# Kernel optimization log

Measured on AMD Instinct MI355X. Metric: run time of the kernel, lower is better.

The kernel has to match this reference:

```python
import jax, jax.numpy as jnp
import numpy as np

B, S, D = 2048, 200, 128  # batch, history length, embedding dim
H = 64                    # attention_units[0]

def setup_inputs() -> dict:
    key = jax.random.key(0)
    k1, k2, k3, k4, k5 = jax.random.split(key, 5)
    return {
        "target_item": jax.random.normal(k1, (B, D), dtype=jnp.float32),
        "history_sequence": jax.random.normal(k2, (B, S, D), dtype=jnp.float32),
        "mask": jax.random.randint(k3, (B, S), 0, 2, dtype=jnp.int32),
        "W1": jax.random.normal(k4, (4 * D, H), dtype=jnp.float32) * (1.0 / np.sqrt(4 * D)),
        "b1": jnp.zeros((H,), dtype=jnp.float32),
        "W2": jax.random.normal(k5, (H, 1), dtype=jnp.float32) * (1.0 / np.sqrt(H)),
        "b2": jnp.zeros((1,), dtype=jnp.float32),
    }

def reference(target_item, history_sequence, mask, W1, b1, W2, b2):
    b, s, d = history_sequence.shape
    t = jnp.broadcast_to(target_item[:, None, :], (b, s, d))  # [B,S,D]
    # concat(target, history, diff, product) -> [B,S,4D]
    x = jnp.concatenate(
        [t, history_sequence, t - history_sequence, t * history_sequence], axis=-1)
    h = jax.nn.relu(x @ W1 + b1)          # [B,S,H]
    w = (h @ W2 + b2)[..., 0]             # [B,S]
    m = mask.astype(w.dtype)
    w = w * m                              # zero out padded positions (pre-softmax, as in source)
    w = w + (-1e9) * (1.0 - m)             # mask for softmax
    w = jax.nn.softmax(w, axis=-1)
    return jnp.einsum('bs,bsd->bd', w, history_sequence)  # [B,D]
```

## Files before the change

### kernel.cpp

```cpp
#include <hip/hip_runtime.h>
#include <hip/hip_bf16.h>

typedef __attribute__((ext_vector_type(8))) short bf16x8;
typedef __attribute__((ext_vector_type(4))) float f32x4;

#define B_ 2048
#define S_ 200
#define D_ 128
#define H_ 64
#define LOG2E 1.44269504f
#define TR 16
#define TB 8192

#define WS_AC 0u
#define WS_WB 32768u

static __device__ __forceinline__ short f2bf_hw(float f) {
    return (short)__builtin_bit_cast(unsigned short, __float2bfloat16(f));
}

static __device__ __forceinline__ void gload16(const void* g, void* l) {
    __builtin_amdgcn_global_load_lds(
        (const __attribute__((address_space(1))) unsigned int*)g,
        (__attribute__((address_space(3))) unsigned int*)l, 16, 0, 0);
}

__global__ __launch_bounds__(128)
void prep_fold(const float* __restrict__ W1, char* __restrict__ ws)
{
    const int n = blockIdx.x;
    const int k = threadIdx.x;
    float a = W1[k * H_ + n];
    float b = W1[(128 + k) * H_ + n];
    float c = W1[(256 + k) * H_ + n];
    float d = W1[(384 + k) * H_ + n];
    ((float*)(ws + WS_AC))[k * 64 + n] = a + c;
    char* img = ws + WS_WB;
    const int sw = (n & 7) << 4;
    const int kk = k >> 3, e2 = (k & 7) * 2;
    *(short*)(img + n * 512 + ((kk * 16) ^ sw) + e2)        = f2bf_hw(b - c);
    *(short*)(img + n * 512 + (((16 + kk) * 16) ^ sw) + e2) = f2bf_hw(d);
}

__global__ __launch_bounds__(256) __attribute__((amdgpu_waves_per_eu(1, 1)))
void din_fused(const float* __restrict__ tgt, const float* __restrict__ hist,
               const int* __restrict__ mask, const float* __restrict__ W2,
               const float* __restrict__ b1, const char* __restrict__ ws,
               float* __restrict__ out)
{
    __shared__ __align__(16) char L[139264];
    const int tid  = threadIdx.x;
    const int lane = tid & 63;
    const int wv   = tid >> 6;
    const int b    = blockIdx.x * 4 + wv;
    const int lo   = lane & 15;
    const int hi   = lane >> 4;
    char* Lm = L + 32768 + wv * 26624;

    {
        const char* wsrc = ws + WS_WB + wv * 8192 + (size_t)lane * 16u;
        #pragma unroll
        for (int i = 0; i < 8; ++i)
            gload16(wsrc + i * 1024, L + wv * 8192 + i * 1024);
    }

    f32x4 w2v[4];
    #pragma unroll
    for (int ng = 0; ng < 4; ++ng) {
        f32x4 wl = *(const f32x4*)(W2 + ng * 16 + hi * 4);
        w2v[ng] = (f32x4){wl[0] * LOG2E, wl[1] * LOG2E, wl[2] * LOG2E, wl[3] * LOG2E};
    }
    f32x4 tp0[4], tp1[4];
    #pragma unroll
    for (int ks = 0; ks < 4; ++ks) {
        tp0[ks] = *(const f32x4*)(tgt + (size_t)b * D_ + ks * 32 + hi * 8);
        tp1[ks] = *(const f32x4*)(tgt + (size_t)b * D_ + ks * 32 + hi * 8 + 4);
    }

    int* lst = (int*)(Lm + 1024);
    int cnt = 0, uni = 0;
    {
        const int* mp = mask + (size_t)b * S_;
        int last = 0;
        #pragma unroll
        for (int c = 0; c < 4; ++c) {
            int s = c * 64 + lane;
            int m = (s < S_) ? mp[s] : 0;
            unsigned long long bal = __ballot(m != 0);
            if (m) lst[cnt + __builtin_popcountll(bal & ((1ull << lane) - 1ull))] = s;
            if (bal) last = c * 64 + (63 - __builtin_clzll(bal));
            cnt += __builtin_popcountll(bal);
        }
        if (cnt == 0) { uni = 1; cnt = S_; }
        for (int p = cnt + lane; p < 208; p += 64) lst[p] = uni ? (S_ - 1) : last;
        if (uni)
            for (int p = lane; p < S_; p += 64) lst[p] = p;
    }

    {
        const float* ak = (const float*)(ws + WS_AC) + lane;
        const float* tb = tgt + (size_t)b * D_;
        float ta = 0.f;
        #pragma unroll 16
        for (int d = 0; d < 128; ++d)
            ta = fmaf(tb[d], ak[d * 64], ta);
        ta += b1[lane];
        *(float*)(Lm + 512 + lane * 4) = ta;
    }
    f32x4 tav[4];
    #pragma unroll
    for (int ng = 0; ng < 4; ++ng)
        tav[ng] = *(const f32x4*)(Lm + 512 + (ng * 16 + hi * 4) * 4);

    asm volatile("s_waitcnt vmcnt(0)" ::: "memory");
    __syncthreads();

    const int nt = (cnt + 15) >> 4;
    const int* ll = (const int*)(Lm + 1024);

    int abase[4], akoff[8];
    #pragma unroll
    for (int ng = 0; ng < 4; ++ng) abase[ng] = (ng * 16 + lo) * 512;
    #pragma unroll
    for (int ks = 0; ks < 8; ++ks) akoff[ks] = (ks * 64 + hi * 16) ^ ((lo & 7) << 4);
    bf16x8 bfH[4][4];
    #pragma unroll
    for (int ks = 0; ks < 4; ++ks)
        #pragma unroll
        for (int ng = 0; ng < 4; ++ng)
            bfH[ks][ng] = *(const bf16x8*)(L + abase[ng] + akoff[ks]);

    const int rb = (lo * 512 + hi * 32) ^ ((lo & 7) << 4);
    char* BB0 = Lm + 2048;
    char* BB1 = Lm + 2048 + TB;
    char* BB2 = Lm + 2048 + 2 * TB;

    const char* hb = (const char*)hist + (size_t)b * (S_ * D_ * 4);
    const int cp = (lane & 31) * 16;
    const int h5 = lane >> 5;
    auto stage = [&](int t, char* bufp) {
        #pragma unroll
        for (int i = 0; i < 8; ++i) {
            int r = 2 * i + h5;
            int rr = ll[t * 16 + r];
            gload16(hb + (size_t)rr * 512 + (cp ^ ((r & 7) << 4)), bufp + i * 1024);
        }
    };
    stage(0, BB0);
    stage(nt > 1 ? 1 : 0, BB1);
    stage(nt > 2 ? 2 : nt - 1, BB2);

    float o[4][8];
    #pragma unroll
    for (int ks = 0; ks < 4; ++ks)
        #pragma unroll
        for (int e = 0; e < 8; ++e) o[ks][e] = 0.f;
    float l = 0.f, mx = -1e30f;

    #pragma unroll 1
    for (int t = 0; t < nt; ++t) {
        char* buf = (t % 3 == 0) ? BB0 : (t % 3 == 1) ? BB1 : BB2;
        asm volatile("s_waitcnt vmcnt(16)" ::: "memory");
        __builtin_amdgcn_sched_barrier(0);
        f32x4 h0[4], h1[4];
        #pragma unroll
        for (int ks = 0; ks < 4; ++ks) {
            int o4 = rb + ks * 128;
            h0[ks] = *(const f32x4*)(buf + o4);
            h1[ks] = *(const f32x4*)(buf + (o4 ^ 16));
        }
        asm volatile("s_waitcnt lgkmcnt(0)" ::: "memory");
        __builtin_amdgcn_sched_barrier(0);
        if (t + 1 < nt) {
            int ts = t + 3; if (ts > nt - 1) ts = nt - 1;
            stage(ts, buf);
        }
        f32x4 acc[4];
        #pragma unroll
        for (int ng = 0; ng < 4; ++ng) acc[ng] = (f32x4){0.f, 0.f, 0.f, 0.f};
        #pragma unroll
        for (int ks = 0; ks < 4; ++ks) {
            bf16x8 bh, bt;
            #pragma unroll
            for (int e = 0; e < 4; ++e) {
                bh[e]     = f2bf_hw(h0[ks][e]);
                bh[e + 4] = f2bf_hw(h1[ks][e]);
                bt[e]     = f2bf_hw(tp0[ks][e] * h0[ks][e]);
                bt[e + 4] = f2bf_hw(tp1[ks][e] * h1[ks][e]);
            }
            #pragma unroll
            for (int ng = 0; ng < 4; ++ng)
                acc[ng] = __builtin_amdgcn_mfma_f32_16x16x32_bf16(bfH[ks][ng], bh, acc[ng], 0, 0, 0);
            #pragma unroll
            for (int ng = 0; ng < 4; ++ng) {
                bf16x8 afd = *(const bf16x8*)(L + abase[ng] + akoff[ks + 4]);
                acc[ng] = __builtin_amdgcn_mfma_f32_16x16x32_bf16(afd, bt, acc[ng], 0, 0, 0);
            }
        }
        float s0 = 0.f, s1 = 0.f, s2 = 0.f, s3 = 0.f;
        #pragma unroll
        for (int e = 0; e < 4; ++e) {
            s0 = fmaf(fmaxf(acc[0][e] + tav[0][e], 0.f), w2v[0][e], s0);
            s1 = fmaf(fmaxf(acc[1][e] + tav[1][e], 0.f), w2v[1][e], s1);
            s2 = fmaf(fmaxf(acc[2][e] + tav[2][e], 0.f), w2v[2][e], s2);
            s3 = fmaf(fmaxf(acc[3][e] + tav[3][e], 0.f), w2v[3][e], s3);
        }
        float sum = (s0 + s1) + (s2 + s3);
        sum += __shfl_xor(sum, 16);
        sum += __shfl_xor(sum, 32);
        const bool valid = (t * 16 + lo) < cnt;
        float lg = uni ? (valid ? 0.f : -1e30f) : (valid ? sum : -1e30f);
        float tm = lg;
        tm = fmaxf(tm, __shfl_xor(tm, 1));
        tm = fmaxf(tm, __shfl_xor(tm, 2));
        tm = fmaxf(tm, __shfl_xor(tm, 4));
        tm = fmaxf(tm, __shfl_xor(tm, 8));
        if (tm > mx + 11.5f) {
            float rsc = exp2f(mx - tm);
            #pragma unroll
            for (int ks = 0; ks < 4; ++ks)
                #pragma unroll
                for (int e = 0; e < 8; ++e) o[ks][e] *= rsc;
            l *= rsc;
            mx = tm;
        }
        float p = valid ? exp2f(lg - mx) : 0.f;
        l += p;
        #pragma unroll
        for (int ks = 0; ks < 4; ++ks) {
            o[ks][0] = fmaf(p, h0[ks][0], o[ks][0]);
            o[ks][1] = fmaf(p, h0[ks][1], o[ks][1]);
            o[ks][2] = fmaf(p, h0[ks][2], o[ks][2]);
            o[ks][3] = fmaf(p, h0[ks][3], o[ks][3]);
            o[ks][4] = fmaf(p, h1[ks][0], o[ks][4]);
            o[ks][5] = fmaf(p, h1[ks][1], o[ks][5]);
            o[ks][6] = fmaf(p, h1[ks][2], o[ks][6]);
            o[ks][7] = fmaf(p, h1[ks][3], o[ks][7]);
        }
    }

    #pragma unroll
    for (int ks = 0; ks < 4; ++ks)
        #pragma unroll
        for (int e = 0; e < 8; ++e) {
            float v = o[ks][e];
            v += __shfl_xor(v, 1);
            v += __shfl_xor(v, 2);
            v += __shfl_xor(v, 4);
            v += __shfl_xor(v, 8);
            o[ks][e] = v;
        }
    l += __shfl_xor(l, 1);
    l += __shfl_xor(l, 2);
    l += __shfl_xor(l, 4);
    l += __shfl_xor(l, 8);

    const float inv = 1.0f / l;
    if (lo == 0) {
        float* op = out + (size_t)b * D_ + hi * 8;
        #pragma unroll
        for (int ks = 0; ks < 4; ++ks) {
            *(f32x4*)(op + ks * 32)     = (f32x4){o[ks][0] * inv, o[ks][1] * inv,
                                                  o[ks][2] * inv, o[ks][3] * inv};
            *(f32x4*)(op + ks * 32 + 4) = (f32x4){o[ks][4] * inv, o[ks][5] * inv,
                                                  o[ks][6] * inv, o[ks][7] * inv};
        }
    }
}

extern "C" void kernel_launch(void* const* d_in, const int* in_sizes, int n_in,
                              void* d_out, int out_size, void* d_ws, size_t ws_size,
                              hipStream_t stream) {
    const float* tgt  = (const float*)d_in[0];
    const float* hist = (const float*)d_in[1];
    const int*   mask = (const int*)d_in[2];
    const float* W1   = (const float*)d_in[3];
    const float* b1   = (const float*)d_in[4];
    const float* W2   = (const float*)d_in[5];
    const float* b2   = (const float*)d_in[6];
    (void)b2;
    float* out = (float*)d_out;
    char* ws = (char*)d_ws;

    prep_fold<<<64, 128, 0, stream>>>(W1, ws);
    din_fused<<<B_ / 4, 256, 0, stream>>>(tgt, hist, mask, W2, b1, ws, out);
}
```

Before: 51.34 us.

## Replace LDS triple-buffered history staging with register double-buffering and higher occupancy

The history rows are no longer staged into LDS through async global-to-LDS loads with a three-buffer ring. Each thread now loads its gathered row slice straight into registers, double-buffered across two tile sets. This shrinks shared memory per block and allows 8 waves per block with two blocks per CU instead of one wave per EU. The W1 fragments for the history half are reread from LDS each tile instead of held in registers, which saves registers at the cost of extra LDS reads. Latency hiding now depends on occupancy and register prefetch rather than an explicit async pipeline.

New measurement: 166.9 us. +225.1%, slower.

```diff
diff --git a/kernel.cpp b/kernel.cpp
--- a/kernel.cpp
+++ b/kernel.cpp
@@ -9,11 +9,12 @@
 #define D_ 128
 #define H_ 64
 #define LOG2E 1.44269504f
-#define TR 16
-#define TB 8192
 
 #define WS_AC 0u
 #define WS_WB 32768u
+
+#define L_META 32768
+#define M_STRIDE 1536
 
 static __device__ __forceinline__ short f2bf_hw(float f) {
     return (short)__builtin_bit_cast(unsigned short, __float2bfloat16(f));
@@ -42,26 +43,26 @@
     *(short*)(img + n * 512 + (((16 + kk) * 16) ^ sw) + e2) = f2bf_hw(d);
 }
 
-__global__ __launch_bounds__(256) __attribute__((amdgpu_waves_per_eu(1, 1)))
+__global__ __launch_bounds__(512, 2)
 void din_fused(const float* __restrict__ tgt, const float* __restrict__ hist,
                const int* __restrict__ mask, const float* __restrict__ W2,
                const float* __restrict__ b1, const char* __restrict__ ws,
                float* __restrict__ out)
 {
-    __shared__ __align__(16) char L[139264];
+    __shared__ __align__(16) char L[L_META + 8 * M_STRIDE];
     const int tid  = threadIdx.x;
     const int lane = tid & 63;
     const int wv   = tid >> 6;
-    const int b    = blockIdx.x * 4 + wv;
+    const int b    = blockIdx.x * 8 + wv;
     const int lo   = lane & 15;
     const int hi   = lane >> 4;
-    char* Lm = L + 32768 + wv * 26624;
+    char* Lm = L + L_META + wv * M_STRIDE;
 
     {
-        const char* wsrc = ws + WS_WB + wv * 8192 + (size_t)lane * 16u;
-        #pragma unroll
-        for (int i = 0; i < 8; ++i)
-            gload16(wsrc + i * 1024, L + wv * 8192 + i * 1024);
+        const char* wsrc = ws + WS_WB + wv * 4096 + (size_t)lane * 16u;
+        #pragma unroll
+        for (int i = 0; i < 4; ++i)
+            gload16(wsrc + i * 1024, L + wv * 4096 + i * 1024);
     }
 
     f32x4 w2v[4];
@@ -77,7 +78,7 @@
         tp1[ks] = *(const f32x4*)(tgt + (size_t)b * D_ + ks * 32 + hi * 8 + 4);
     }
 
-    int* lst = (int*)(Lm + 1024);
+    int* lst = (int*)(Lm + 256);
     int cnt = 0, uni = 0;
     {
         const int* mp = mask + (size_t)b * S_;
@@ -104,51 +105,34 @@
         #pragma unroll 16
         for (int d = 0; d < 128; ++d)
             ta = fmaf(tb[d], ak[d * 64], ta);
-        ta += b1[lane];
-        *(float*)(Lm + 512 + lane * 4) = ta;
+        *(float*)(Lm + lane * 4) = ta + b1[lane];
     }
     f32x4 tav[4];
     #pragma unroll
     for (int ng = 0; ng < 4; ++ng)
-        tav[ng] = *(const f32x4*)(Lm + 512 + (ng * 16 + hi * 4) * 4);
+        tav[ng] = *(const f32x4*)(Lm + (ng * 16 + hi * 4) * 4);
 
     asm volatile("s_waitcnt vmcnt(0)" ::: "memory");
     __syncthreads();
 
     const int nt = (cnt + 15) >> 4;
-    const int* ll = (const int*)(Lm + 1024);
+    const int* ll = (const int*)(Lm + 256);
 
     int abase[4], akoff[8];
     #pragma unroll
     for (int ng = 0; ng < 4; ++ng) abase[ng] = (ng * 16 + lo) * 512;
     #pragma unroll
     for (int ks = 0; ks < 8; ++ks) akoff[ks] = (ks * 64 + hi * 16) ^ ((lo & 7) << 4);
-    bf16x8 bfH[4][4];
-    #pragma unroll
-    for (int ks = 0; ks < 4; ++ks)
-        #pragma unroll
-        for (int ng = 0; ng < 4; ++ng)
-            bfH[ks][ng] = *(const bf16x8*)(L + abase[ng] + akoff[ks]);
-
-    const int rb = (lo * 512 + hi * 32) ^ ((lo & 7) << 4);
-    char* BB0 = Lm + 2048;
-    char* BB1 = Lm + 2048 + TB;
-    char* BB2 = Lm + 2048 + 2 * TB;
-
-    const char* hb = (const char*)hist + (size_t)b * (S_ * D_ * 4);
-    const int cp = (lane & 31) * 16;
-    const int h5 = lane >> 5;
-    auto stage = [&](int t, char* bufp) {
-        #pragma unroll
-        for (int i = 0; i < 8; ++i) {
-            int r = 2 * i + h5;
-            int rr = ll[t * 16 + r];
-            gload16(hb + (size_t)rr * 512 + (cp ^ ((r & 7) << 4)), bufp + i * 1024);
+
+    auto loadt = [&](f32x4 (&st)[4][2], int t) {
+        int row = ll[t * 16 + lo];
+        const float* hp = hist + ((size_t)b * S_ + row) * D_ + hi * 8;
+        #pragma unroll
+        for (int ks = 0; ks < 4; ++ks) {
+            st[ks][0] = *(const f32x4*)(hp + ks * 32);
+            st[ks][1] = *(const f32x4*)(hp + ks * 32 + 4);
         }
     };
-    stage(0, BB0);
-    stage(nt > 1 ? 1 : 0, BB1);
-    stage(nt > 2 ? 2 : nt - 1, BB2);
 
     float o[4][8];
     #pragma unroll
@@ -157,24 +141,7 @@
         for (int e = 0; e < 8; ++e) o[ks][e] = 0.f;
     float l = 0.f, mx = -1e30f;
 
-    #pragma unroll 1
-    for (int t = 0; t < nt; ++t) {
-        char* buf = (t % 3 == 0) ? BB0 : (t % 3 == 1) ? BB1 : BB2;
-        asm volatile("s_waitcnt vmcnt(16)" ::: "memory");
-        __builtin_amdgcn_sched_barrier(0);
-        f32x4 h0[4], h1[4];
-        #pragma unroll
-        for (int ks = 0; ks < 4; ++ks) {
-            int o4 = rb + ks * 128;
-            h0[ks] = *(const f32x4*)(buf + o4);
-            h1[ks] = *(const f32x4*)(buf + (o4 ^ 16));
-        }
-        asm volatile("s_waitcnt lgkmcnt(0)" ::: "memory");
-        __builtin_amdgcn_sched_barrier(0);
-        if (t + 1 < nt) {
-            int ts = t + 3; if (ts > nt - 1) ts = nt - 1;
-            stage(ts, buf);
-        }
+    auto compt = [&](f32x4 (&st)[4][2], int t) {
         f32x4 acc[4];
         #pragma unroll
         for (int ng = 0; ng < 4; ++ng) acc[ng] = (f32x4){0.f, 0.f, 0.f, 0.f};
@@ -183,14 +150,16 @@
             bf16x8 bh, bt;
             #pragma unroll
             for (int e = 0; e < 4; ++e) {
-                bh[e]     = f2bf_hw(h0[ks][e]);
-                bh[e + 4] = f2bf_hw(h1[ks][e]);
-                bt[e]     = f2bf_hw(tp0[ks][e] * h0[ks][e]);
-                bt[e + 4] = f2bf_hw(tp1[ks][e] * h1[ks][e]);
+                bh[e]     = f2bf_hw(st[ks][0][e]);
+                bh[e + 4] = f2bf_hw(st[ks][1][e]);
+                bt[e]     = f2bf_hw(tp0[ks][e] * st[ks][0][e]);
+                bt[e + 4] = f2bf_hw(tp1[ks][e] * st[ks][1][e]);
             }
             #pragma unroll
-            for (int ng = 0; ng < 4; ++ng)
-                acc[ng] = __builtin_amdgcn_mfma_f32_16x16x32_bf16(bfH[ks][ng], bh, acc[ng], 0, 0, 0);
+            for (int ng = 0; ng < 4; ++ng) {
+                bf16x8 afh = *(const bf16x8*)(L + abase[ng] + akoff[ks]);
+                acc[ng] = __builtin_amdgcn_mfma_f32_16x16x32_bf16(afh, bh, acc[ng], 0, 0, 0);
+            }
             #pragma unroll
             for (int ng = 0; ng < 4; ++ng) {
                 bf16x8 afd = *(const bf16x8*)(L + abase[ng] + akoff[ks + 4]);
@@ -228,16 +197,29 @@
         l += p;
         #pragma unroll
         for (int ks = 0; ks < 4; ++ks) {
-            o[ks][0] = fmaf(p, h0[ks][0], o[ks][0]);
-            o[ks][1] = fmaf(p, h0[ks][1], o[ks][1]);
-            o[ks][2] = fmaf(p, h0[ks][2], o[ks][2]);
-            o[ks][3] = fmaf(p, h0[ks][3], o[ks][3]);
-            o[ks][4] = fmaf(p, h1[ks][0], o[ks][4]);
-            o[ks][5] = fmaf(p, h1[ks][1], o[ks][5]);
-            o[ks][6] = fmaf(p, h1[ks][2], o[ks][6]);
-            o[ks][7] = fmaf(p, h1[ks][3], o[ks][7]);
-        }
-    }
+            o[ks][0] = fmaf(p, st[ks][0][0], o[ks][0]);
+            o[ks][1] = fmaf(p, st[ks][0][1], o[ks][1]);
+            o[ks][2] = fmaf(p, st[ks][0][2], o[ks][2]);
+            o[ks][3] = fmaf(p, st[ks][0][3], o[ks][3]);
+            o[ks][4] = fmaf(p, st[ks][1][0], o[ks][4]);
+            o[ks][5] = fmaf(p, st[ks][1][1], o[ks][5]);
+            o[ks][6] = fmaf(p, st[ks][1][2], o[ks][6]);
+            o[ks][7] = fmaf(p, st[ks][1][3], o[ks][7]);
+        }
+    };
+
+    f32x4 stA[4][2], stB[4][2];
+    loadt(stA, 0);
+    if (nt > 1) loadt(stB, 1);
+    int t = 0;
+    #pragma unroll 1
+    for (; t + 1 < nt; t += 2) {
+        compt(stA, t);
+        if (t + 2 < nt) loadt(stA, t + 2);
+        compt(stB, t + 1);
+        if (t + 3 < nt) loadt(stB, t + 3);
+    }
+    if (t < nt) compt(stA, t);
 
     #pragma unroll
     for (int ks = 0; ks < 4; ++ks)
@@ -283,5 +265,5 @@
     char* ws = (char*)d_ws;
 
     prep_fold<<<64, 128, 0, stream>>>(W1, ws);
-    din_fused<<<B_ / 4, 256, 0, stream>>>(tgt, hist, mask, W2, b1, ws, out);
-}
+    din_fused<<<B_ / 8, 512, 0, stream>>>(tgt, hist, mask, W2, b1, ws, out);
+}
```
